# Kernel tuning notes

Measured on AMD Instinct MI355X. Metric: run time of the kernel, lower is better.

The kernel has to match this reference:

```python
import jax, jax.numpy as jnp
import numpy as np

PAD = 0  # vocab[PADDING]
T, B, S, E, H, V = 32, 32, 200, 512, 512, 50000


def setup_inputs() -> dict:
    key = jax.random.key(0)
    ks = jax.random.split(key, 16)
    u = lambda k, sh, s: jax.random.uniform(k, sh, jnp.float32, -s, s)
    lstm_s = 1.0 / np.sqrt(H)
    inp = {}
    inp["tgt_in"] = jax.random.randint(ks[0], (T, B), 0, V)
    inp["tgt_out"] = jax.random.randint(ks[1], (T, B), 0, V)
    inp["src_lens"] = jax.random.randint(ks[2], (B,), S // 2, S + 1)  # valid lengths >= 1
    inp["src_encodings"] = jax.random.normal(ks[3], (B, S, H), jnp.float32) * 0.1
    inp["last_state"] = jax.random.normal(ks[4], (1, B, H), jnp.float32) * 0.1
    inp["last_cell"] = jax.random.normal(ks[5], (1, B, H), jnp.float32) * 0.1
    inp["embed_table"] = jax.random.normal(ks[6], (V, E), jnp.float32) * 0.02
    in_sz = E + H  # input_feed=True
    inp["W_ih"] = u(ks[7], (4 * H, in_sz), lstm_s)
    inp["W_hh"] = u(ks[8], (4 * H, H), lstm_s)
    inp["b_ih"] = u(ks[9], (4 * H,), lstm_s)
    inp["b_hh"] = u(ks[10], (4 * H,), lstm_s)
    inp["W_attn"] = u(ks[11], (H, 2 * H), 1.0 / np.sqrt(2 * H))  # linear_out, no bias (dot attn)
    inp["W_gen"] = u(ks[12], (H, E + 2 * H), 1.0 / np.sqrt(E + 2 * H))
    inp["b_gen"] = u(ks[13], (H,), 1.0 / np.sqrt(E + 2 * H))
    inp["W_read"] = u(ks[14], (V, H), 1.0 / np.sqrt(H))  # readout, bias=False
    return inp


def reference(tgt_in, tgt_out, src_lens, src_encodings, last_state, last_cell,
              embed_table, W_ih, W_hh, b_ih, b_hh, W_attn, W_gen, b_gen, W_read):
    Bn = tgt_in.shape[1]
    Sn = src_encodings.shape[1]
    Hn = last_state.shape[-1]
    emb = embed_table[tgt_in]  # (T,B,E)
    len_mask = jnp.arange(Sn)[None, :] < src_lens[:, None]  # (B,S)
    h0 = last_state[0]
    c0 = last_cell[0]
    att0 = jnp.zeros((Bn, Hn), emb.dtype)  # att_tm1 init

    def step(carry, y_emb):
        h, c, att = carry
        x = jnp.concatenate([y_emb, att], axis=-1)  # input feed: (B,E+H)
        g = x @ W_ih.T + h @ W_hh.T + b_ih + b_hh  # (B,4H), torch gate order i,f,g,o
        i, f, gg, o = jnp.split(g, 4, axis=-1)
        c_new = jax.nn.sigmoid(f) * c + jax.nn.sigmoid(i) * jnp.tanh(gg)
        h_new = jax.nn.sigmoid(o) * jnp.tanh(c_new)
        # GlobalAttention (dot, softmax), query = last_state
        scores = jnp.einsum('bh,bsh->bs', h_new, src_encodings)  # (B,S)
        scores = jnp.where(len_mask, scores, -jnp.inf)
        alpha = jax.nn.softmax(scores, axis=-1)  # (B,S)
        ctx = jnp.einsum('bs,bsh->bh', alpha, src_encodings)  # (B,H)
        att_t = jnp.tanh(jnp.concatenate([ctx, h_new], axis=-1) @ W_attn.T)  # (B,H)
        cat_final = jnp.concatenate([y_emb, h_new, att_t], axis=-1)  # (B,E+2H)
        dec = jnp.tanh(cat_final @ W_gen.T + b_gen)  # (B,H)
        return (h_new, c_new, att_t), (dec, alpha)

    _, (decs, alphas) = jax.lax.scan(step, (h0, c0, att0), emb)  # decs: (T,B,H)
    logits = decs @ W_read.T  # (T,B,V)
    words_log_prob = jax.nn.log_softmax(logits, axis=-1)
    ys = jnp.argmax(words_log_prob, axis=-1)  # (T,B)
    words_mask = (tgt_out != PAD).astype(words_log_prob.dtype)
    word_losses = -jnp.take_along_axis(words_log_prob, tgt_out[..., None], axis=-1)[..., 0] * words_mask
    return word_losses, ys
```

## Files before the change

kernel.cpp:

```cpp
#include <hip/hip_runtime.h>
#include <math.h>

#define T_ 32
#define B_ 32
#define S_ 200
#define E_ 512
#define H_ 512
#define V_ 50000
#define VP_ 50176
#define G4_ 2048
#define NCH 196

using bf16x8 = __attribute__((ext_vector_type(8))) __bf16;
using f32x4  = __attribute__((ext_vector_type(4))) float;

__device__ __forceinline__ float sigf(float x) { return 1.f / (1.f + expf(-x)); }

__device__ __forceinline__ unsigned short f2bf(float v) {
    unsigned int x = __float_as_uint(v);
    return (unsigned short)((x + 0x7FFFu + ((x >> 16) & 1u)) >> 16);
}
__device__ __forceinline__ float bf2f(unsigned short b) {
    return __uint_as_float(((unsigned int)b) << 16);
}

__device__ __forceinline__ void async16(void* lds, const void* g) {
    __builtin_amdgcn_global_load_lds(
        (const __attribute__((address_space(1))) unsigned int*)g,
        (__attribute__((address_space(3))) unsigned int*)lds, 16, 0, 0);
}

__device__ __forceinline__ void g_store(float* p, float v) {
    __hip_atomic_store(p, v, __ATOMIC_RELAXED, __HIP_MEMORY_SCOPE_AGENT);
}
__device__ __forceinline__ float g_load(const float* p) {
    return __hip_atomic_load(p, __ATOMIC_RELAXED, __HIP_MEMORY_SCOPE_AGENT);
}

__device__ __forceinline__ void full_sync(int* bar, int ep) {
    __syncthreads();
    if (threadIdx.x == 0) {
        const int g = blockIdx.x & 7;
        int a = __hip_atomic_fetch_add(&bar[g * 32], 1, __ATOMIC_RELAXED, __HIP_MEMORY_SCOPE_AGENT);
        if (a == ep * 32 + 31) {
            int q = __hip_atomic_fetch_add(&bar[256], 1, __ATOMIC_RELAXED, __HIP_MEMORY_SCOPE_AGENT);
            if (q == ep * 8 + 7) {
                #pragma unroll
                for (int i = 0; i < 8; i++)
                    __hip_atomic_store(&bar[288 + i * 32], ep + 1, __ATOMIC_RELAXED, __HIP_MEMORY_SCOPE_AGENT);
            }
        }
        while (__hip_atomic_load(&bar[288 + g * 32], __ATOMIC_RELAXED, __HIP_MEMORY_SCOPE_AGENT) < ep + 1)
            __builtin_amdgcn_s_sleep(1);
    }
    __syncthreads();
}

__device__ __forceinline__ void sub_sync(int* bar, int bb, int t) {
    __syncthreads();
    if (threadIdx.x == 0) {
        __hip_atomic_fetch_add(&bar[544 + bb * 32], 1, __ATOMIC_RELAXED, __HIP_MEMORY_SCOPE_AGENT);
        while (__hip_atomic_load(&bar[544 + bb * 32], __ATOMIC_RELAXED, __HIP_MEMORY_SCOPE_AGENT) < (t + 1) * 8)
            __builtin_amdgcn_s_sleep(1);
    }
    __syncthreads();
}

__global__ __launch_bounds__(256) void k_init(const float* __restrict__ last_state,
                                              float* __restrict__ xT) {
    const int f = blockIdx.x * 256 + threadIdx.x;
    xT[f] = 0.f;
    const int k = f >> 5, b = f & 31;
    xT[32768 + f] = last_state[b * 512 + k];
}

#define CVT_R0 819200
#define CVT_R1 (CVT_R0 + 65536)
#define CVT_R2 (CVT_R1 + 262144)
#define CVT_R3 (CVT_R2 + 131072)
#define CVT_R4 (CVT_R3 + 196608)
__global__ __launch_bounds__(256) void k_cvt(const float* __restrict__ src,
                                             const float* __restrict__ Wattn,
                                             const float* __restrict__ Wih,
                                             const float* __restrict__ emb,
                                             const float* __restrict__ Wgen,
                                             const int* __restrict__ tgt_in,
                                             unsigned short* __restrict__ sh,
                                             unsigned short* __restrict__ sl,
                                             unsigned short* __restrict__ wah,
                                             unsigned short* __restrict__ wal,
                                             unsigned short* __restrict__ wih_h,
                                             unsigned short* __restrict__ wih_l,
                                             unsigned short* __restrict__ eh,
                                             unsigned short* __restrict__ el,
                                             unsigned short* __restrict__ wgh,
                                             unsigned short* __restrict__ wgl) {
    const int u = blockIdx.x * 256 + threadIdx.x;
    if (u >= CVT_R4) return;
    const float* sp;
    unsigned short *dh_, *dl_;
    size_t doff;
    if (u < CVT_R0) {
        sp = src + (size_t)u * 4;
        dh_ = sh; dl_ = sl; doff = (size_t)u * 4;
    } else if (u < CVT_R1) {
        const int idx = u - CVT_R0;
        const int k4 = idx & 127, n = idx >> 7;
        sp = Wattn + (size_t)n * 1024 + k4 * 4;
        dh_ = wah; dl_ = wal; doff = (size_t)n * 512 + k4 * 4;
    } else if (u < CVT_R2) {
        const int idx = u - CVT_R1;
        const int k4 = idx & 127, j = idx >> 7;
        sp = Wih + (size_t)j * 1024 + k4 * 4;
        dh_ = wih_h; dl_ = wih_l; doff = (size_t)j * 512 + k4 * 4;
    } else if (u < CVT_R3) {
        const int idx = u - CVT_R2;
        const int k4 = idx & 127, m = idx >> 7;
        sp = emb + (size_t)tgt_in[m] * 512 + k4 * 4;
        dh_ = eh; dl_ = el; doff = (size_t)m * 512 + k4 * 4;
    } else {
        const int idx = u - CVT_R3;
        const int n = idx / 384, k4 = idx - n * 384;
        sp = Wgen + (size_t)n * 1536 + k4 * 4;
        dh_ = wgh; dl_ = wgl; doff = (size_t)n * 1536 + k4 * 4;
    }
    const float4 v = *(const float4*)sp;
    const float vv[4] = {v.x, v.y, v.z, v.w};
    unsigned int hb[4], lb[4];
    #pragma unroll
    for (int e = 0; e < 4; e++) {
        hb[e] = f2bf(vv[e]);
        lb[e] = f2bf(vv[e] - bf2f((unsigned short)hb[e]));
    }
    *(uint2*)(dh_ + doff) = make_uint2(hb[0] | (hb[1] << 16), hb[2] | (hb[3] << 16));
    *(uint2*)(dl_ + doff) = make_uint2(lb[0] | (lb[1] << 16), lb[2] | (lb[3] << 16));
}

__global__ __launch_bounds__(256) void k_gbt(const unsigned short* __restrict__ Ah,
                                             const unsigned short* __restrict__ Al,
                                             const unsigned short* __restrict__ Bh,
                                             const unsigned short* __restrict__ Bl,
                                             const float* __restrict__ bih,
                                             const float* __restrict__ bhh,
                                             float* __restrict__ out,
                                             int nbn, int mode) {
    __shared__ __align__(16) unsigned short BhL[4][256][8];
    __shared__ __align__(16) unsigned short BlL[4][256][8];
    __shared__ __align__(16) unsigned short AhL[4][64][8];
    __shared__ __align__(16) unsigned short AlL[4][64][8];
    const int m0 = (blockIdx.x / nbn) * 64;
    const int n0 = (blockIdx.x % nbn) * 256;
    const int tid = threadIdx.x;
    const int lane = tid & 63, wid = tid >> 6;
    const int wr = wid >> 1, wc = wid & 1;
    const int l15 = lane & 15, lk = lane >> 4;

    f32x4 acc[2][8];
    #pragma unroll
    for (int mt = 0; mt < 2; mt++)
        #pragma unroll
        for (int nt = 0; nt < 8; nt++) acc[mt][nt] = {0.f, 0.f, 0.f, 0.f};

    for (int kc = 0; kc < 512; kc += 32) {
        {
            #pragma unroll
            for (int g = 0; g < 4; g++) {
                const size_t bo = (size_t)(n0 + tid) * 512 + kc + g * 8;
                *(uint4*)&BhL[g][tid][0] = *(const uint4*)(Bh + bo);
                *(uint4*)&BlL[g][tid][0] = *(const uint4*)(Bl + bo);
            }
        }
        {
            const int row = tid >> 2, g = tid & 3;
            const size_t ao = (size_t)(m0 + row) * 512 + kc + g * 8;
            *(uint4*)&AhL[g][row][0] = *(const uint4*)(Ah + ao);
            *(uint4*)&AlL[g][row][0] = *(const uint4*)(Al + ao);
        }
        __syncthreads();
        {
            bf16x8 afh[2], afl[2];
            #pragma unroll
            for (int mt = 0; mt < 2; mt++) {
                const int r = wr * 32 + mt * 16 + l15;
                afh[mt] = *(const bf16x8*)&AhL[lk][r][0];
                afl[mt] = *(const bf16x8*)&AlL[lk][r][0];
            }
            #pragma unroll
            for (int nt = 0; nt < 8; nt++) {
                const int nn = wc * 128 + nt * 16 + l15;
                bf16x8 bh = *(const bf16x8*)&BhL[lk][nn][0];
                bf16x8 bl = *(const bf16x8*)&BlL[lk][nn][0];
                #pragma unroll
                for (int mt = 0; mt < 2; mt++) {
                    acc[mt][nt] = __builtin_amdgcn_mfma_f32_16x16x32_bf16(afh[mt], bh, acc[mt][nt], 0, 0, 0);
                    acc[mt][nt] = __builtin_amdgcn_mfma_f32_16x16x32_bf16(afl[mt], bh, acc[mt][nt], 0, 0, 0);
                    acc[mt][nt] = __builtin_amdgcn_mfma_f32_16x16x32_bf16(afh[mt], bl, acc[mt][nt], 0, 0, 0);
                }
            }
        }
        __syncthreads();
    }
    #pragma unroll
    for (int mt = 0; mt < 2; mt++)
        #pragma unroll
        for (int reg = 0; reg < 4; reg++) {
            const int row = m0 + wr * 32 + mt * 16 + lk * 4 + reg;
            #pragma unroll
            for (int nt = 0; nt < 8; nt++) {
                const int col = n0 + wc * 128 + nt * 16 + l15;
                const float v = acc[mt][nt][reg];
                if (mode == 0) out[(size_t)row * 512 + col] = v;
                else           out[(size_t)col * 1024 + row] = v + bih[col] + bhh[col];
            }
        }
}

__global__ __launch_bounds__(256) void k_gbt_dec(const unsigned short* __restrict__ eh,
                                                 const unsigned short* __restrict__ el,
                                                 const unsigned short* __restrict__ hh,
                                                 const unsigned short* __restrict__ hl,
                                                 const unsigned short* __restrict__ ath,
                                                 const unsigned short* __restrict__ atl,
                                                 const unsigned short* __restrict__ wgh,
                                                 const unsigned short* __restrict__ wgl,
                                                 const float* __restrict__ bgen,
                                                 unsigned short* __restrict__ dhk,
                                                 unsigned short* __restrict__ dlk) {
    __shared__ __align__(16) unsigned short BhL[4][256][8];
    __shared__ __align__(16) unsigned short BlL[4][256][8];
    __shared__ __align__(16) unsigned short AhL[4][64][8];
    __shared__ __align__(16) unsigned short AlL[4][64][8];
    const int m0 = (blockIdx.x >> 1) * 64;
    const int n0 = (blockIdx.x & 1) * 256;
    const int tid = threadIdx.x;
    const int lane = tid & 63, wid = tid >> 6;
    const int wr = wid >> 1, wc = wid & 1;
    const int l15 = lane & 15, lk = lane >> 4;

    f32x4 acc[2][8];
    #pragma unroll
    for (int mt = 0; mt < 2; mt++)
        #pragma unroll
        for (int nt = 0; nt < 8; nt++) acc[mt][nt] = {0.f, 0.f, 0.f, 0.f};

    for (int kc = 0; kc < 1536; kc += 32) {
        const unsigned short *Ahp, *Alp;
        int ko;
        if (kc < 512)       { Ahp = eh;  Alp = el;  ko = kc; }
        else if (kc < 1024) { Ahp = hh;  Alp = hl;  ko = kc - 512; }
        else                { Ahp = ath; Alp = atl; ko = kc - 1024; }
        {
            #pragma unroll
            for (int g = 0; g < 4; g++) {
                const size_t bo = (size_t)(n0 + tid) * 1536 + kc + g * 8;
                *(uint4*)&BhL[g][tid][0] = *(const uint4*)(wgh + bo);
                *(uint4*)&BlL[g][tid][0] = *(const uint4*)(wgl + bo);
            }
        }
        {
            const int row = tid >> 2, g = tid & 3;
            const size_t ao = (size_t)(m0 + row) * 512 + ko + g * 8;
            *(uint4*)&AhL[g][row][0] = *(const uint4*)(Ahp + ao);
            *(uint4*)&AlL[g][row][0] = *(const uint4*)(Alp + ao);
        }
        __syncthreads();
        {
            bf16x8 afh[2], afl[2];
            #pragma unroll
            for (int mt = 0; mt < 2; mt++) {
                const int r = wr * 32 + mt * 16 + l15;
                afh[mt] = *(const bf16x8*)&AhL[lk][r][0];
                afl[mt] = *(const bf16x8*)&AlL[lk][r][0];
            }
            #pragma unroll
            for (int nt = 0; nt < 8; nt++) {
                const int nn = wc * 128 + nt * 16 + l15;
                bf16x8 bh = *(const bf16x8*)&BhL[lk][nn][0];
                bf16x8 bl = *(const bf16x8*)&BlL[lk][nn][0];
                #pragma unroll
                for (int mt = 0; mt < 2; mt++) {
                    acc[mt][nt] = __builtin_amdgcn_mfma_f32_16x16x32_bf16(afh[mt], bh, acc[mt][nt], 0, 0, 0);
                    acc[mt][nt] = __builtin_amdgcn_mfma_f32_16x16x32_bf16(afl[mt], bh, acc[mt][nt], 0, 0, 0);
                    acc[mt][nt] = __builtin_amdgcn_mfma_f32_16x16x32_bf16(afh[mt], bl, acc[mt][nt], 0, 0, 0);
                }
            }
        }
        __syncthreads();
    }
    #pragma unroll
    for (int mt = 0; mt < 2; mt++)
        #pragma unroll
        for (int reg = 0; reg < 4; reg++) {
            const int row = m0 + wr * 32 + mt * 16 + lk * 4 + reg;
            #pragma unroll
            for (int nt = 0; nt < 8; nt++) {
                const int col = n0 + wc * 128 + nt * 16 + l15;
                const float v = tanhf(acc[mt][nt][reg] + bgen[col]);
                const unsigned short hb = f2bf(v);
                const unsigned short lb = f2bf(v - bf2f(hb));
                const size_t ca = (size_t)(col >> 5) * 32768 + (size_t)(row >> 6) * 2048
                                + (size_t)(row & 63) * 32 + (col & 31);
                dhk[ca] = hb;
                dlk[ca] = lb;
            }
        }
}

__global__ __launch_bounds__(256) void k_g0(const int* __restrict__ tgt_in,
                                            const float* __restrict__ emb,
                                            const float* __restrict__ Wih,
                                            const float* __restrict__ bih,
                                            const float* __restrict__ bhh,
                                            float* __restrict__ G0T) {
    __shared__ float a_s[32][66];
    __shared__ float w_s[32][130];
    const int tid = threadIdx.x;
    const int m0 = blockIdx.x * 64, n0 = blockIdx.y * 128;
    const int mq = tid >> 5, nq = tid & 31;
    float acc[8][4] = {};
    for (int k0 = 0; k0 < 512; k0 += 32) {
        {
            const int mm = tid >> 2, kq = tid & 3, kk = kq * 8;
            const float* row = emb + (size_t)tgt_in[m0 + mm] * E_ + k0 + kk;
            float4 v0 = *(const float4*)(row);
            float4 v1 = *(const float4*)(row + 4);
            a_s[kk + 0][mm] = v0.x; a_s[kk + 1][mm] = v0.y;
            a_s[kk + 2][mm] = v0.z; a_s[kk + 3][mm] = v0.w;
            a_s[kk + 4][mm] = v1.x; a_s[kk + 5][mm] = v1.y;
            a_s[kk + 6][mm] = v1.z; a_s[kk + 7][mm] = v1.w;
        }
        {
            const int nn = tid >> 1, kq = tid & 1, kk = kq * 16;
            const float* row = Wih + (size_t)(n0 + nn) * 1024 + k0 + kk;
            #pragma unroll
            for (int u = 0; u < 4; u++) {
                float4 v = *(const float4*)(row + u * 4);
                w_s[kk + u * 4 + 0][nn] = v.x; w_s[kk + u * 4 + 1][nn] = v.y;
                w_s[kk + u * 4 + 2][nn] = v.z; w_s[kk + u * 4 + 3][nn] = v.w;
            }
        }
        __syncthreads();
        for (int k = 0; k < 32; k++) {
            float a[8], wv[4];
            #pragma unroll
            for (int i = 0; i < 8; i++) a[i] = a_s[k][mq + 8 * i];
            #pragma unroll
            for (int p = 0; p < 4; p++) wv[p] = w_s[k][nq + 32 * p];
            #pragma unroll
            for (int i = 0; i < 8; i++)
                #pragma unroll
                for (int p = 0; p < 4; p++) acc[i][p] += a[i] * wv[p];
        }
        __syncthreads();
    }
    #pragma unroll
    for (int i = 0; i < 8; i++) {
        const int m = m0 + mq + 8 * i;
        #pragma unroll
        for (int p = 0; p < 4; p++) {
            const int n = n0 + nq + 32 * p;
            G0T[(size_t)n * 1024 + m] = acc[i][p] + bih[n] + bhh[n];
        }
    }
}

__global__ __launch_bounds__(256) void k_u(const float* __restrict__ src,
                                           const float* __restrict__ Wattn,
                                           float* __restrict__ U) {
    __shared__ float a_s[32][66];
    __shared__ float w_s[32][130];
    const int tid = threadIdx.x;
    const int m0 = blockIdx.x * 64, n0 = blockIdx.y * 128;
    const int mq = tid >> 5, nq = tid & 31;
    float acc[8][4] = {};
    for (int k0 = 0; k0 < 512; k0 += 32) {
        {
            const int mm = tid >> 2, kq = tid & 3, kk = kq * 8;
            const float* row = src + (size_t)(m0 + mm) * 512 + k0 + kk;
            float4 v0 = *(const float4*)(row);
            float4 v1 = *(const float4*)(row + 4);
            a_s[kk + 0][mm] = v0.x; a_s[kk + 1][mm] = v0.y;
            a_s[kk + 2][mm] = v0.z; a_s[kk + 3][mm] = v0.w;
            a_s[kk + 4][mm] = v1.x; a_s[kk + 5][mm] = v1.y;
            a_s[kk + 6][mm] = v1.z; a_s[kk + 7][mm] = v1.w;
        }
        {
            const int nn = tid >> 1, kq = tid & 1, kk = kq * 16;
            const float* row = Wattn + (size_t)(n0 + nn) * 1024 + k0 + kk;
            #pragma unroll
            for (int u = 0; u < 4; u++) {
                float4 v = *(const float4*)(row + u * 4);
                w_s[kk + u * 4 + 0][nn] = v.x; w_s[kk + u * 4 + 1][nn] = v.y;
                w_s[kk + u * 4 + 2][nn] = v.z; w_s[kk + u * 4 + 3][nn] = v.w;
            }
        }
        __syncthreads();
        for (int k = 0; k < 32; k++) {
            float a[8], wv[4];
            #pragma unroll
            for (int i = 0; i < 8; i++) a[i] = a_s[k][mq + 8 * i];
            #pragma unroll
            for (int p = 0; p < 4; p++) wv[p] = w_s[k][nq + 32 * p];
            #pragma unroll
            for (int i = 0; i < 8; i++)
                #pragma unroll
                for (int p = 0; p < 4; p++) acc[i][p] += a[i] * wv[p];
        }
        __syncthreads();
    }
    #pragma unroll
    for (int i = 0; i < 8; i++) {
        const int m = m0 + mq + 8 * i;
        #pragma unroll
        for (int p = 0; p < 4; p++)
            U[(size_t)m * 512 + n0 + nq + 32 * p] = acc[i][p];
    }
}

__global__ __launch_bounds__(256) void k_tr(const float* __restrict__ Wattn,
                                            float* __restrict__ WaRT) {
    __shared__ float t_s[32][33];
    const int tid = threadIdx.x;
    const int bx = blockIdx.x, by = blockIdx.y;
    {
        const int jj = tid >> 3, kq = (tid & 7) * 4;
        float4 v = *(const float4*)(Wattn + (size_t)(by * 32 + jj) * 1024 + 512 + bx * 32 + kq);
        t_s[jj][kq + 0] = v.x; t_s[jj][kq + 1] = v.y;
        t_s[jj][kq + 2] = v.z; t_s[jj][kq + 3] = v.w;
    }
    __syncthreads();
    {
        const int kk = tid >> 3, jq = (tid & 7) * 4;
        float4 w;
        w.x = t_s[jq + 0][kk]; w.y = t_s[jq + 1][kk];
        w.z = t_s[jq + 2][kk]; w.w = t_s[jq + 3][kk];
        *(float4*)(WaRT + (size_t)(bx * 32 + kk) * 512 + by * 32 + jq) = w;
    }
}

__global__ __launch_bounds__(256) void k_wconv(const float* __restrict__ Wread,
                                               unsigned short* __restrict__ whk,
                                               unsigned short* __restrict__ wlk) {
    const size_t q = (size_t)blockIdx.x * 256 + threadIdx.x;
    const size_t k8 = q * 8;
    const int n = (int)(k8 >> 9);
    const int k = (int)(k8 & 511);
    if (n >= VP_) return;
    uint4 h4, l4;
    if (n < V_) {
        float4 p0 = *(const float4*)(Wread + (size_t)n * 512 + k);
        float4 p1 = *(const float4*)(Wread + (size_t)n * 512 + k + 4);
        float v[8] = {p0.x, p0.y, p0.z, p0.w, p1.x, p1.y, p1.z, p1.w};
        unsigned int hb[8], lb[8];
        #pragma unroll
        for (int e = 0; e < 8; e++) {
            hb[e] = f2bf(v[e]);
            lb[e] = f2bf(v[e] - bf2f((unsigned short)hb[e]));
        }
        h4 = make_uint4(hb[0] | (hb[1] << 16), hb[2] | (hb[3] << 16),
                        hb[4] | (hb[5] << 16), hb[6] | (hb[7] << 16));
        l4 = make_uint4(lb[0] | (lb[1] << 16), lb[2] | (lb[3] << 16),
                        lb[4] | (lb[5] << 16), lb[6] | (lb[7] << 16));
    } else {
        h4 = make_uint4(0, 0, 0, 0);
        l4 = make_uint4(0, 0, 0, 0);
    }
    const int lk = (k >> 3) & 3;
    const size_t dst = (size_t)(k >> 5) * ((size_t)VP_ * 32) + (size_t)n * 32
                     + (size_t)((lk ^ ((n >> 1) & 3)) * 8);
    *(uint4*)(whk + dst) = h4;
    *(uint4*)(wlk + dst) = l4;
}

__global__ __launch_bounds__(512) void k_scan(const float* __restrict__ G0T,
                                              const float* __restrict__ U,
                                              const float* __restrict__ WaRT,
                                              const float* __restrict__ Wih,
                                              const float* __restrict__ Whh,
                                              const float* __restrict__ src,
                                              const int* __restrict__ lens,
                                              const float* __restrict__ last_cell,
                                              float* __restrict__ xT,
                                              float* __restrict__ h_b,
                                              float* __restrict__ scb,
                                              float* __restrict__ h_hist,
                                              float* __restrict__ att_hist,
                                              unsigned short* __restrict__ hh,
                                              unsigned short* __restrict__ hl,
                                              unsigned short* __restrict__ ath,
                                              unsigned short* __restrict__ atl,
                                              int pre,
                                              int* __restrict__ bar) {
    __shared__ float Wl[8 * 1024];
    __shared__ float Ul[200 * 64];
    __shared__ float red_s[2048];
    __shared__ float gate_s[256];
    __shared__ float h_s[512];
    __shared__ float al[256];
    __shared__ float pr[512];

    const int blk = blockIdx.x, tid = threadIdx.x;
    const int u0 = blk * 2;
    const int bb = blk & 31, p = blk >> 5;

    for (int f = tid; f < 2048; f += 512) {
        const int r = f >> 8, k = (f & 255) * 4;
        const int j = (r >> 1) * 512 + u0 + (r & 1);
        float4 v;
        if (k < 512) v = *(const float4*)(Wih + (size_t)j * 1024 + 512 + k);
        else         v = *(const float4*)(Whh + (size_t)j * 512 + (k - 512));
        *(float4*)&Wl[r * 1024 + k] = v;
    }
    for (int f = tid; f < 3200; f += 512) {
        const int s = f >> 4, q = (f & 15) * 4;
        *(float4*)&Ul[s * 64 + q] = *(const float4*)(U + ((size_t)bb * S_ + s) * 512 + p * 64 + q);
    }
    float creg = (tid < 64) ? last_cell[(tid & 31) * 512 + u0 + (tid >> 5)] : 0.f;
    __syncthreads();

    const int w = tid >> 6, lane = tid & 63;
    const int hf = lane >> 5, b = lane & 31;
    const int len = lens[bb];

    for (int t = 0; t < T_; t++) {
        {
            const int hoff = ((t + 1) & 1) * 512;
            const int kbase = w * 128 + hf * 64;
            const float* xp = (kbase < 512)
                ? (xT + (size_t)kbase * 32 + b)
                : (xT + (size_t)(512 + hoff + (kbase - 512)) * 32 + b);
            float acc[8] = {};
            #pragma unroll
            for (int kk = 0; kk < 64; kk += 8) {
                float xv[8];
                #pragma unroll
                for (int i = 0; i < 8; i++)
                    xv[i] = g_load(xp + (size_t)(kk + i) * 32);
                #pragma unroll
                for (int r = 0; r < 8; r++) {
                    const float* wr = &Wl[r * 1024 + kbase + kk];
                    float s0 = xv[0] * wr[0] + xv[1] * wr[1] + xv[2] * wr[2] + xv[3] * wr[3];
                    float s1 = xv[4] * wr[4] + xv[5] * wr[5] + xv[6] * wr[6] + xv[7] * wr[7];
                    acc[r] += s0 + s1;
                }
            }
            #pragma unroll
            for (int r = 0; r < 8; r++) acc[r] += __shfl_xor(acc[r], 32);
            if (hf == 0) {
                #pragma unroll
                for (int r = 0; r < 8; r++) red_s[w * 256 + r * 32 + b] = acc[r];
            }
            __syncthreads();
            if (tid < 256) {
                const int r = tid >> 5, b2 = tid & 31;
                const int j = (r >> 1) * 512 + u0 + (r & 1);
                float g = G0T[(size_t)j * 1024 + t * 32 + b2];
                #pragma unroll
                for (int ww = 0; ww < 8; ww++) g += red_s[ww * 256 + r * 32 + b2];
                gate_s[r * 32 + b2] = g;
            }
            __syncthreads();
            if (tid < 64) {
                const int ui = tid >> 5, b2 = tid & 31, u = u0 + ui;
                const float gi = gate_s[(0 + ui) * 32 + b2];
                const float gf = gate_s[(2 + ui) * 32 + b2];
                const float gg = gate_s[(4 + ui) * 32 + b2];
                const float go = gate_s[(6 + ui) * 32 + b2];
                const float cn = sigf(gf) * creg + sigf(gi) * tanhf(gg);
                const float hn = sigf(go) * tanhf(cn);
                creg = cn;
                g_store(&xT[(size_t)(512 + (t & 1) * 512 + u) * 32 + b2], hn);
                g_store(&h_b[b2 * 512 + u], hn);
                h_hist[((size_t)t * B_ + b2) * 512 + u] = hn;
                if (pre) {
                    const unsigned short hb2 = f2bf(hn);
                    const size_t ho = ((size_t)t * B_ + b2) * 512 + u;
                    hh[ho] = hb2;
                    hl[ho] = f2bf(hn - bf2f(hb2));
                }
            }
        }
        full_sync(bar, 2 * t);

        {
            h_s[tid] = g_load(&h_b[bb * 512 + tid]);
            __syncthreads();
            for (int i = w; i < 25; i += 8) {
                const int s = p * 25 + i;
                const float* sr = src + ((size_t)bb * S_ + s) * 512;
                const float4 x0 = *(const float4*)(sr + lane * 4);
                const float4 x1 = *(const float4*)(sr + 256 + lane * 4);
                const float4 h0 = *(const float4*)(&h_s[lane * 4]);
                const float4 h1 = *(const float4*)(&h_s[256 + lane * 4]);
                float a = x0.x * h0.x + x0.y * h0.y + x0.z * h0.z + x0.w * h0.w
                        + x1.x * h1.x + x1.y * h1.y + x1.z * h1.z + x1.w * h1.w;
                #pragma unroll
                for (int mk = 1; mk < 64; mk <<= 1) a += __shfl_xor(a, mk);
                if (lane == 0) g_store(&scb[bb * 256 + s], (s < len) ? a : -INFINITY);
            }
        }
        sub_sync(bar, bb, t);

        {
            if (tid < 64) {
                const float v0 = g_load(&scb[bb * 256 + tid]);
                const float v1 = g_load(&scb[bb * 256 + 64 + tid]);
                const float v2 = g_load(&scb[bb * 256 + 128 + tid]);
                const float v3 = (tid < 8) ? g_load(&scb[bb * 256 + 192 + tid]) : -INFINITY;
                float m = fmaxf(fmaxf(v0, v1), fmaxf(v2, v3));
                #pragma unroll
                for (int mk = 1; mk < 64; mk <<= 1) m = fmaxf(m, __shfl_xor(m, mk));
                const float e0 = expf(v0 - m), e1 = expf(v1 - m), e2 = expf(v2 - m);
                const float e3 = (tid < 8) ? expf(v3 - m) : 0.f;
                float sum = (e0 + e1) + (e2 + e3);
                #pragma unroll
                for (int mk = 1; mk < 64; mk <<= 1) sum += __shfl_xor(sum, mk);
                const float inv = 1.f / sum;
                al[tid] = e0 * inv; al[64 + tid] = e1 * inv; al[128 + tid] = e2 * inv;
                if (tid < 8) al[192 + tid] = e3 * inv;
            }
            __syncthreads();
            const int jl = tid & 63, sg = tid >> 6;
            float uacc = 0.f;
            #pragma unroll 5
            for (int s = sg * 25; s < sg * 25 + 25; s++)
                uacc += al[s] * Ul[s * 64 + jl];
            const float* wc0 = WaRT + (size_t)(sg * 64) * 512 + p * 64 + jl;
            const float* hp = &h_s[sg * 64];
            float c0 = 0.f, c1 = 0.f;
            #pragma unroll 8
            for (int kk = 0; kk < 64; kk += 2) {
                c0 += hp[kk] * wc0[(size_t)kk * 512];
                c1 += hp[kk + 1] * wc0[(size_t)(kk + 1) * 512];
            }
            pr[tid] = uacc + c0 + c1;
            __syncthreads();
            if (tid < 64) {
                float tot = 0.f;
                #pragma unroll
                for (int sgg = 0; sgg < 8; sgg++) tot += pr[sgg * 64 + tid];
                const float a = tanhf(tot);
                g_store(&xT[(size_t)(p * 64 + tid) * 32 + bb], a);
                att_hist[((size_t)t * B_ + bb) * 512 + p * 64 + tid] = a;
                if (pre) {
                    const unsigned short ab = f2bf(a);
                    const size_t ao = ((size_t)t * B_ + bb) * 512 + p * 64 + tid;
                    ath[ao] = ab;
                    atl[ao] = f2bf(a - bf2f(ab));
                }
            }
        }
        full_sync(bar, 2 * t + 1);
    }
}

__global__ __launch_bounds__(256) void k_dec(const int* __restrict__ tgt_in,
                                             const float* __restrict__ emb,
                                             const float* __restrict__ h_hist,
                                             const float* __restrict__ att_hist,
                                             const float* __restrict__ Wgen,
                                             const float* __restrict__ bgen,
                                             unsigned short* __restrict__ dh,
                                             unsigned short* __restrict__ dl) {
    __shared__ float a_s[32][66];
    __shared__ float w_s[32][130];
    const int tid = threadIdx.x;
    const int m0 = blockIdx.x * 64, n0 = blockIdx.y * 128;
    const int mq = tid >> 5, nq = tid & 31;
    float acc[8][4] = {};
    for (int k0 = 0; k0 < 1536; k0 += 32) {
        {
            const int mm = tid >> 2, kq = tid & 3, kk = kq * 8;
            const int m = m0 + mm;
            const float* row;
            if (k0 < 512)       row = emb + (size_t)tgt_in[m] * E_ + k0;
            else if (k0 < 1024) row = h_hist + (size_t)m * 512 + (k0 - 512);
            else                row = att_hist + (size_t)m * 512 + (k0 - 1024);
            row += kk;
            float4 v0 = *(const float4*)(row);
            float4 v1 = *(const float4*)(row + 4);
            a_s[kk + 0][mm] = v0.x; a_s[kk + 1][mm] = v0.y;
            a_s[kk + 2][mm] = v0.z; a_s[kk + 3][mm] = v0.w;
            a_s[kk + 4][mm] = v1.x; a_s[kk + 5][mm] = v1.y;
            a_s[kk + 6][mm] = v1.z; a_s[kk + 7][mm] = v1.w;
        }
        {
            const int nn = tid >> 1, kq = tid & 1, kk = kq * 16;
            const float* row = Wgen + (size_t)(n0 + nn) * 1536 + k0 + kk;
            #pragma unroll
            for (int u = 0; u < 4; u++) {
                float4 v = *(const float4*)(row + u * 4);
                w_s[kk + u * 4 + 0][nn] = v.x; w_s[kk + u * 4 + 1][nn] = v.y;
                w_s[kk + u * 4 + 2][nn] = v.z; w_s[kk + u * 4 + 3][nn] = v.w;
            }
        }
        __syncthreads();
        for (int k = 0; k < 32; k++) {
            float a[8], wv[4];
            #pragma unroll
            for (int i = 0; i < 8; i++) a[i] = a_s[k][mq + 8 * i];
            #pragma unroll
            for (int pq = 0; pq < 4; pq++) wv[pq] = w_s[k][nq + 32 * pq];
            #pragma unroll
            for (int i = 0; i < 8; i++)
                #pragma unroll
                for (int pq = 0; pq < 4; pq++) acc[i][pq] += a[i] * wv[pq];
        }
        __syncthreads();
    }
    #pragma unroll
    for (int i = 0; i < 8; i++) {
        const int m = m0 + mq + 8 * i;
        #pragma unroll
        for (int pq = 0; pq < 4; pq++) {
            const int n = n0 + nq + 32 * pq;
            const float v = tanhf(acc[i][pq] + bgen[n]);
            const unsigned short hb = f2bf(v);
            dh[(size_t)m * 512 + n] = hb;
            dl[(size_t)m * 512 + n] = f2bf(v - bf2f(hb));
        }
    }
}

__global__ __launch_bounds__(256) void k_read_pre(const unsigned short* __restrict__ dhk,
                                                  const unsigned short* __restrict__ dlk,
                                                  const unsigned short* __restrict__ whk,
                                                  const unsigned short* __restrict__ wlk,
                                                  const int* __restrict__ tgt_out,
                                                  float4* __restrict__ part,
                                                  float* __restrict__ tgt_logit) {
    __shared__ __align__(16) unsigned short BhL[8192];
    __shared__ __align__(16) unsigned short BlL[8192];
    __shared__ float ep_max[64][2];
    __shared__ int   ep_idx[64][2];
    __shared__ float ep_fin[64];
    __shared__ int   ep_fidx[64];
    __shared__ float ep_sum[64][2];

    const int xcd = blockIdx.x & 7;
    const int idx = blockIdx.x >> 3;
    const int mi  = idx & 15;
    const int group = idx >> 4;
    const int ch = group * 8 + xcd;
    if (ch >= NCH) return;
    const int m0 = mi * 64, n0 = ch * 256;

    const int tid = threadIdx.x;
    const int lane = tid & 63, wid = tid >> 6;
    const int wr = wid >> 1, wc = wid & 1;
    const int l15 = lane & 15, lk = lane >> 4;

    f32x4 acc[2][8];
    #pragma unroll
    for (int mt = 0; mt < 2; mt++)
        #pragma unroll
        for (int nt = 0; nt < 8; nt++) acc[mt][nt] = {0.f, 0.f, 0.f, 0.f};

    const unsigned short* bh_src = whk + (size_t)n0 * 32;
    const unsigned short* bl_src = wlk + (size_t)n0 * 32;
    const unsigned short* ah_base = dhk + (size_t)(m0 >> 6) * 2048 + lk * 8;
    const unsigned short* al_base = dlk + (size_t)(m0 >> 6) * 2048 + lk * 8;

    for (int kc = 0; kc < 16; kc++) {
        {
            const size_t cb = (size_t)kc * ((size_t)VP_ * 32);
            const char* gh = (const char*)(bh_src + cb);
            const char* gl = (const char*)(bl_src + cb);
            #pragma unroll
            for (int c = 0; c < 4; c++) {
                const int ob = wid * 4096 + c * 1024;
                async16((char*)BhL + ob, gh + ob + lane * 16);
                async16((char*)BlL + ob, gl + ob + lane * 16);
            }
        }
        bf16x8 afh[2], afl[2];
        {
            const unsigned short* ah = ah_base + (size_t)kc * 32768;
            const unsigned short* al = al_base + (size_t)kc * 32768;
            #pragma unroll
            for (int mt = 0; mt < 2; mt++) {
                const int r = wr * 32 + mt * 16 + l15;
                afh[mt] = *(const bf16x8*)(ah + r * 32);
                afl[mt] = *(const bf16x8*)(al + r * 32);
            }
        }
        __syncthreads();
        #pragma unroll
        for (int nt = 0; nt < 8; nt++) {
            const int nn = wc * 128 + nt * 16 + l15;
            const int bo = nn * 32 + ((lk ^ ((nn >> 1) & 3)) * 8);
            bf16x8 bh = *(const bf16x8*)&BhL[bo];
            bf16x8 bl = *(const bf16x8*)&BlL[bo];
            #pragma unroll
            for (int mt = 0; mt < 2; mt++) {
                acc[mt][nt] = __builtin_amdgcn_mfma_f32_16x16x32_bf16(afh[mt], bh, acc[mt][nt], 0, 0, 0);
                acc[mt][nt] = __builtin_amdgcn_mfma_f32_16x16x32_bf16(afl[mt], bh, acc[mt][nt], 0, 0, 0);
                acc[mt][nt] = __builtin_amdgcn_mfma_f32_16x16x32_bf16(afh[mt], bl, acc[mt][nt], 0, 0, 0);
            }
        }
        __syncthreads();
    }

    #pragma unroll
    for (int mt = 0; mt < 2; mt++)
        #pragma unroll
        for (int reg = 0; reg < 4; reg++) {
            float bv = -INFINITY; int bi = 0x7fffffff;
            #pragma unroll
            for (int nt = 0; nt < 8; nt++) {
                const int n = n0 + wc * 128 + nt * 16 + l15;
                const float v = (n < V_) ? acc[mt][nt][reg] : -INFINITY;
                if (v > bv || (v == bv && n < bi)) { bv = v; bi = n; }
            }
            #pragma unroll
            for (int mk = 1; mk < 16; mk <<= 1) {
                const float ov = __shfl_xor(bv, mk);
                const int oi = __shfl_xor(bi, mk);
                if (ov > bv || (ov == bv && oi < bi)) { bv = ov; bi = oi; }
            }
            if (l15 == 0) {
                const int rl = wr * 32 + mt * 16 + lk * 4 + reg;
                ep_max[rl][wc] = bv; ep_idx[rl][wc] = bi;
            }
        }
    __syncthreads();
    if (tid < 64) {
        const float a = ep_max[tid][0], b = ep_max[tid][1];
        const int ia = ep_idx[tid][0], ib = ep_idx[tid][1];
        const bool tb = (b > a) || (b == a && ib < ia);
        ep_fin[tid] = tb ? b : a; ep_fidx[tid] = tb ? ib : ia;
    }
    __syncthreads();
    #pragma unroll
    for (int mt = 0; mt < 2; mt++)
        #pragma unroll
        for (int reg = 0; reg < 4; reg++) {
            const int rl = wr * 32 + mt * 16 + lk * 4 + reg;
            const float M = ep_fin[rl];
            const int rel = tgt_out[m0 + rl] - n0;
            float se = 0.f;
            #pragma unroll
            for (int nt = 0; nt < 8; nt++) {
                const int nl = wc * 128 + nt * 16 + l15;
                if (n0 + nl < V_) {
                    const float v = acc[mt][nt][reg];
                    se += expf(v - M);
                    if (nl == rel) tgt_logit[m0 + rl] = v;
                }
            }
            #pragma unroll
            for (int mk = 1; mk < 16; mk <<= 1) se += __shfl_xor(se, mk);
            if (l15 == 0) ep_sum[rl][wc] = se;
        }
    __syncthreads();
    if (tid < 64) {
        part[(size_t)(m0 + tid) * NCH + ch] =
            make_float4(ep_fin[tid], ep_sum[tid][0] + ep_sum[tid][1],
                        __int_as_float(ep_fidx[tid]), 0.f);
    }
}

__global__ __launch_bounds__(256) void k_read(const unsigned short* __restrict__ dh,
                                              const unsigned short* __restrict__ dl,
                                              const float* __restrict__ Wread,
                                              const int* __restrict__ tgt_out,
                                              float4* __restrict__ part,
                                              float* __restrict__ tgt_logit) {
    __shared__ __align__(16) unsigned short Bh[4][256][8];
    __shared__ __align__(16) unsigned short Bl[4][256][8];
    __shared__ __align__(16) unsigned short Ah[4][64][8];
    __shared__ __align__(16) unsigned short Alo[4][64][8];
    __shared__ float ep_max[64][2];
    __shared__ int   ep_idx[64][2];
    __shared__ float ep_fin[64];
    __shared__ int   ep_fidx[64];
    __shared__ float ep_sum[64][2];

    const int xcd = blockIdx.x & 7;
    const int idx = blockIdx.x >> 3;
    const int mi  = idx & 15;
    const int group = idx >> 4;
    const int ch = group * 8 + xcd;
    if (ch >= NCH) return;
    const int m0 = mi * 64, n0 = ch * 256;

    const int tid = threadIdx.x;
    const int lane = tid & 63, wid = tid >> 6;
    const int wr = wid >> 1, wc = wid & 1;
    const int l15 = lane & 15, lk = lane >> 4;

    f32x4 acc[2][8];
    #pragma unroll
    for (int mt = 0; mt < 2; mt++)
        #pragma unroll
        for (int nt = 0; nt < 8; nt++) acc[mt][nt] = {0.f, 0.f, 0.f, 0.f};

    for (int kc = 0; kc < 512; kc += 32) {
        {
            const int n = n0 + tid;
            const float* row = Wread + (size_t)n * 512 + kc;
            #pragma unroll
            for (int g = 0; g < 4; g++) {
                uint4 h4, l4;
                if (n < V_) {
                    float4 p0 = *(const float4*)(row + g * 8);
                    float4 p1 = *(const float4*)(row + g * 8 + 4);
                    float v[8] = {p0.x, p0.y, p0.z, p0.w, p1.x, p1.y, p1.z, p1.w};
                    unsigned int hb[8], lb[8];
                    #pragma unroll
                    for (int e = 0; e < 8; e++) {
                        hb[e] = f2bf(v[e]);
                        lb[e] = f2bf(v[e] - bf2f((unsigned short)hb[e]));
                    }
                    h4 = make_uint4(hb[0] | (hb[1] << 16), hb[2] | (hb[3] << 16),
                                    hb[4] | (hb[5] << 16), hb[6] | (hb[7] << 16));
                    l4 = make_uint4(lb[0] | (lb[1] << 16), lb[2] | (lb[3] << 16),
                                    lb[4] | (lb[5] << 16), lb[6] | (lb[7] << 16));
                } else {
                    h4 = make_uint4(0, 0, 0, 0);
                    l4 = make_uint4(0, 0, 0, 0);
                }
                *(uint4*)&Bh[g][tid][0] = h4;
                *(uint4*)&Bl[g][tid][0] = l4;
            }
        }
        {
            const int row = tid >> 2, g = tid & 3;
            *(uint4*)&Ah[g][row][0]  = *(const uint4*)(dh + (size_t)(m0 + row) * 512 + kc + g * 8);
            *(uint4*)&Alo[g][row][0] = *(const uint4*)(dl + (size_t)(m0 + row) * 512 + kc + g * 8);
        }
        __syncthreads();
        {
            bf16x8 afh[2], afl[2];
            #pragma unroll
            for (int mt = 0; mt < 2; mt++) {
                const int r = wr * 32 + mt * 16 + l15;
                afh[mt] = *(const bf16x8*)&Ah[lk][r][0];
                afl[mt] = *(const bf16x8*)&Alo[lk][r][0];
            }
            #pragma unroll
            for (int nt = 0; nt < 8; nt++) {
                const int nn = wc * 128 + nt * 16 + l15;
                bf16x8 bh = *(const bf16x8*)&Bh[lk][nn][0];
                bf16x8 bl = *(const bf16x8*)&Bl[lk][nn][0];
                #pragma unroll
                for (int mt = 0; mt < 2; mt++) {
                    acc[mt][nt] = __builtin_amdgcn_mfma_f32_16x16x32_bf16(afh[mt], bh, acc[mt][nt], 0, 0, 0);
                    acc[mt][nt] = __builtin_amdgcn_mfma_f32_16x16x32_bf16(afl[mt], bh, acc[mt][nt], 0, 0, 0);
                    acc[mt][nt] = __builtin_amdgcn_mfma_f32_16x16x32_bf16(afh[mt], bl, acc[mt][nt], 0, 0, 0);
                }
            }
        }
        __syncthreads();
    }

    #pragma unroll
    for (int mt = 0; mt < 2; mt++)
        #pragma unroll
        for (int reg = 0; reg < 4; reg++) {
            float bv = -INFINITY; int bi = 0x7fffffff;
            #pragma unroll
            for (int nt = 0; nt < 8; nt++) {
                const int n = n0 + wc * 128 + nt * 16 + l15;
                const float v = (n < V_) ? acc[mt][nt][reg] : -INFINITY;
                if (v > bv || (v == bv && n < bi)) { bv = v; bi = n; }
            }
            #pragma unroll
            for (int mk = 1; mk < 16; mk <<= 1) {
                const float ov = __shfl_xor(bv, mk);
                const int oi = __shfl_xor(bi, mk);
                if (ov > bv || (ov == bv && oi < bi)) { bv = ov; bi = oi; }
            }
            if (l15 == 0) {
                const int rl = wr * 32 + mt * 16 + lk * 4 + reg;
                ep_max[rl][wc] = bv; ep_idx[rl][wc] = bi;
            }
        }
    __syncthreads();
    if (tid < 64) {
        const float a = ep_max[tid][0], b = ep_max[tid][1];
        const int ia = ep_idx[tid][0], ib = ep_idx[tid][1];
        const bool tb = (b > a) || (b == a && ib < ia);
        ep_fin[tid] = tb ? b : a; ep_fidx[tid] = tb ? ib : ia;
    }
    __syncthreads();
    #pragma unroll
    for (int mt = 0; mt < 2; mt++)
        #pragma unroll
        for (int reg = 0; reg < 4; reg++) {
            const int rl = wr * 32 + mt * 16 + lk * 4 + reg;
            const float M = ep_fin[rl];
            const int rel = tgt_out[m0 + rl] - n0;
            float se = 0.f;
            #pragma unroll
            for (int nt = 0; nt < 8; nt++) {
                const int nl = wc * 128 + nt * 16 + l15;
                if (n0 + nl < V_) {
                    const float v = acc[mt][nt][reg];
                    se += expf(v - M);
                    if (nl == rel) tgt_logit[m0 + rl] = v;
                }
            }
            #pragma unroll
            for (int mk = 1; mk < 16; mk <<= 1) se += __shfl_xor(se, mk);
            if (l15 == 0) ep_sum[rl][wc] = se;
        }
    __syncthreads();
    if (tid < 64) {
        part[(size_t)(m0 + tid) * NCH + ch] =
            make_float4(ep_fin[tid], ep_sum[tid][0] + ep_sum[tid][1],
                        __int_as_float(ep_fidx[tid]), 0.f);
    }
}

__global__ __launch_bounds__(256) void k_merge(const float4* __restrict__ part,
                                               const float* __restrict__ tgt_logit,
                                               const int* __restrict__ tgt_out,
                                               float* __restrict__ out) {
    const int tid = threadIdx.x;
    const int w = tid >> 6, lane = tid & 63;
    const int row = blockIdx.x * 4 + w;
    float bm = -INFINITY; int bi = 0x7fffffff;
    for (int ch = lane; ch < NCH; ch += 64) {
        const float4 p = part[(size_t)row * NCH + ch];
        const int pi = __float_as_int(p.z);
        if (p.x > bm || (p.x == bm && pi < bi)) { bm = p.x; bi = pi; }
    }
    #pragma unroll
    for (int mk = 1; mk < 64; mk <<= 1) {
        const float ov = __shfl_xor(bm, mk);
        const int oi = __shfl_xor(bi, mk);
        if (ov > bm || (ov == bm && oi < bi)) { bm = ov; bi = oi; }
    }
    float sum = 0.f;
    for (int ch = lane; ch < NCH; ch += 64) {
        const float4 p = part[(size_t)row * NCH + ch];
        sum += p.y * expf(p.x - bm);
    }
    #pragma unroll
    for (int mk = 1; mk < 64; mk <<= 1) sum += __shfl_xor(sum, mk);
    if (lane == 0) {
        const float lse = bm + logf(sum);
        const int tg = tgt_out[row];
        const float loss = (tg != 0) ? (lse - tgt_logit[row]) : 0.f;
        out[row] = loss;
        out[1024 + row] = (float)bi;
    }
}

extern "C" void kernel_launch(void* const* d_in, const int* in_sizes, int n_in,
                              void* d_out, int out_size, void* d_ws, size_t ws_size,
                              hipStream_t stream) {
    const int* tgt_in = (const int*)d_in[0];
    const int* tgt_out = (const int*)d_in[1];
    const int* src_lens = (const int*)d_in[2];
    const float* src = (const float*)d_in[3];
    const float* last_state = (const float*)d_in[4];
    const float* last_cell = (const float*)d_in[5];
    const float* emb = (const float*)d_in[6];
    const float* Wih = (const float*)d_in[7];
    const float* Whh = (const float*)d_in[8];
    const float* bih = (const float*)d_in[9];
    const float* bhh = (const float*)d_in[10];
    const float* Wattn = (const float*)d_in[11];
    const float* Wgen = (const float*)d_in[12];
    const float* bgen = (const float*)d_in[13];
    const float* Wread = (const float*)d_in[14];
    float* out = (float*)d_out;

    float* ws = (float*)d_ws;
    float* G0T      = ws;
    float* U        = G0T + 2097152;
    float* WaRT     = U + 3276800;
    unsigned short* dh  = (unsigned short*)(WaRT + 262144);
    unsigned short* dl  = dh + 524288;
    unsigned short* dhk = dl + 524288;
    unsigned short* dlk = dhk + 524288;
    float* h_hist   = (float*)(dlk + 524288);
    float* att_hist = h_hist + 524288;
    float* xT       = att_hist + 524288;
    float* h_b      = xT + 49152;
    float* scb      = h_b + 16384;
    float4* part    = (float4*)(scb + 8192);
    float* tgtl     = ((float*)part) + 802816;
    int* bar        = (int*)(tgtl + 1024);
    unsigned short* whk = (unsigned short*)(bar + 2048);
    unsigned short* wlk = whk + (size_t)VP_ * 512;
    unsigned short* sh    = wlk + (size_t)VP_ * 512;
    unsigned short* sl    = sh + 3276800;
    unsigned short* wah   = sl + 3276800;
    unsigned short* wal   = wah + 262144;
    unsigned short* wih_h = wal + 262144;
    unsigned short* wih_l = wih_h + 1048576;
    unsigned short* eh    = wih_l + 1048576;
    unsigned short* el    = eh + 524288;
    unsigned short* wgh   = el + 524288;
    unsigned short* wgl   = wgh + 786432;
    unsigned short* hh    = wgl + 786432;
    unsigned short* hl    = hh + 524288;
    unsigned short* ath   = hl + 524288;
    unsigned short* atl   = ath + 524288;

    const size_t need = (size_t)((char*)(atl + 524288) - (char*)ws);
    const int pre = (ws_size >= need) ? 1 : 0;

    hipMemsetAsync(bar, 0, 8192, stream);

    k_init<<<64, 256, 0, stream>>>(last_state, xT);
    if (pre) {
        k_cvt<<<(CVT_R4 + 255) / 256, 256, 0, stream>>>(src, Wattn, Wih, emb, Wgen, tgt_in,
                                                        sh, sl, wah, wal, wih_h, wih_l,
                                                        eh, el, wgh, wgl);
        k_gbt<<<200, 256, 0, stream>>>(sh, sl, wah, wal, nullptr, nullptr, U, 2, 0);
        k_gbt<<<128, 256, 0, stream>>>(eh, el, wih_h, wih_l, bih, bhh, G0T, 8, 1);
    } else {
        k_g0<<<dim3(16, 16), 256, 0, stream>>>(tgt_in, emb, Wih, bih, bhh, G0T);
        k_u<<<dim3(100, 4), 256, 0, stream>>>(src, Wattn, U);
    }
    k_tr<<<dim3(16, 16), 256, 0, stream>>>(Wattn, WaRT);
    if (pre)
        k_wconv<<<12544, 256, 0, stream>>>(Wread, whk, wlk);

    k_scan<<<256, 512, 0, stream>>>(G0T, U, WaRT, Wih, Whh, src, src_lens, last_cell,
                                    xT, h_b, scb, h_hist, att_hist,
                                    hh, hl, ath, atl, pre, bar);

    if (pre) {
        k_gbt_dec<<<32, 256, 0, stream>>>(eh, el, hh, hl, ath, atl, wgh, wgl, bgen, dhk, dlk);
        k_read_pre<<<3200, 256, 0, stream>>>(dhk, dlk, whk, wlk, tgt_out, part, tgtl);
    } else {
        k_dec<<<dim3(16, 4), 256, 0, stream>>>(tgt_in, emb, h_hist, att_hist, Wgen, bgen, dh, dl);
        k_read<<<3200, 256, 0, stream>>>(dh, dl, Wread, tgt_out, part, tgtl);
    }
    k_merge<<<256, 256, 0, stream>>>(part, tgtl, tgt_out, out);
}
```

Measured before the change: 900.9 us.

## Double-buffer readout weight tiles and split rows across eight waves

The readout GEMM kernel now uses 512 threads (8 waves), each wave owning 16 rows instead of 32, which halves per-thread accumulators. The weight tile loads are double-buffered in shared memory, so the next k-chunk is fetched asynchronously while the current one feeds the MFMAs, and one barrier per iteration is removed. The aim is to hide global-load latency and raise occupancy, at the cost of twice the LDS footprint and more waves re-reading the same B fragments.

```diff
diff --git a/kernel.cpp b/kernel.cpp
--- a/kernel.cpp
+++ b/kernel.cpp
@@ -722,15 +722,15 @@
     }
 }
 
-__global__ __launch_bounds__(256) void k_read_pre(const unsigned short* __restrict__ dhk,
+__global__ __launch_bounds__(512) void k_read_pre(const unsigned short* __restrict__ dhk,
                                                   const unsigned short* __restrict__ dlk,
                                                   const unsigned short* __restrict__ whk,
                                                   const unsigned short* __restrict__ wlk,
                                                   const int* __restrict__ tgt_out,
                                                   float4* __restrict__ part,
                                                   float* __restrict__ tgt_logit) {
-    __shared__ __align__(16) unsigned short BhL[8192];
-    __shared__ __align__(16) unsigned short BlL[8192];
+    __shared__ __align__(16) unsigned short BhL[2][8192];
+    __shared__ __align__(16) unsigned short BlL[2][8192];
     __shared__ float ep_max[64][2];
     __shared__ int   ep_idx[64][2];
     __shared__ float ep_fin[64];
@@ -750,79 +750,81 @@
     const int wr = wid >> 1, wc = wid & 1;
     const int l15 = lane & 15, lk = lane >> 4;
 
-    f32x4 acc[2][8];
-    #pragma unroll
-    for (int mt = 0; mt < 2; mt++)
-        #pragma unroll
-        for (int nt = 0; nt < 8; nt++) acc[mt][nt] = {0.f, 0.f, 0.f, 0.f};
+    f32x4 acc[8];
+    #pragma unroll
+    for (int nt = 0; nt < 8; nt++) acc[nt] = {0.f, 0.f, 0.f, 0.f};
 
     const unsigned short* bh_src = whk + (size_t)n0 * 32;
     const unsigned short* bl_src = wlk + (size_t)n0 * 32;
     const unsigned short* ah_base = dhk + (size_t)(m0 >> 6) * 2048 + lk * 8;
     const unsigned short* al_base = dlk + (size_t)(m0 >> 6) * 2048 + lk * 8;
 
+    {
+        const char* gh = (const char*)bh_src;
+        const char* gl = (const char*)bl_src;
+        #pragma unroll
+        for (int c = 0; c < 2; c++) {
+            const int ob = wid * 2048 + c * 1024;
+            async16((char*)&BhL[0][0] + ob, gh + ob + lane * 16);
+            async16((char*)&BlL[0][0] + ob, gl + ob + lane * 16);
+        }
+    }
+    __syncthreads();
+
     for (int kc = 0; kc < 16; kc++) {
-        {
-            const size_t cb = (size_t)kc * ((size_t)VP_ * 32);
+        const int cur = kc & 1;
+        bf16x8 afh, afl;
+        {
+            const unsigned short* ah = ah_base + (size_t)kc * 32768;
+            const unsigned short* al = al_base + (size_t)kc * 32768;
+            const int r = wr * 16 + l15;
+            afh = *(const bf16x8*)(ah + r * 32);
+            afl = *(const bf16x8*)(al + r * 32);
+        }
+        if (kc < 15) {
+            const size_t cb = (size_t)(kc + 1) * ((size_t)VP_ * 32);
             const char* gh = (const char*)(bh_src + cb);
             const char* gl = (const char*)(bl_src + cb);
             #pragma unroll
-            for (int c = 0; c < 4; c++) {
-                const int ob = wid * 4096 + c * 1024;
-                async16((char*)BhL + ob, gh + ob + lane * 16);
-                async16((char*)BlL + ob, gl + ob + lane * 16);
-            }
-        }
-        bf16x8 afh[2], afl[2];
-        {
-            const unsigned short* ah = ah_base + (size_t)kc * 32768;
-            const unsigned short* al = al_base + (size_t)kc * 32768;
-            #pragma unroll
-            for (int mt = 0; mt < 2; mt++) {
-                const int r = wr * 32 + mt * 16 + l15;
-                afh[mt] = *(const bf16x8*)(ah + r * 32);
-                afl[mt] = *(const bf16x8*)(al + r * 32);
-            }
-        }
-        __syncthreads();
+            for (int c = 0; c < 2; c++) {
+                const int ob = wid * 2048 + c * 1024;
+                async16((char*)&BhL[cur ^ 1][0] + ob, gh + ob + lane * 16);
+                async16((char*)&BlL[cur ^ 1][0] + ob, gl + ob + lane * 16);
+            }
+        }
         #pragma unroll
         for (int nt = 0; nt < 8; nt++) {
             const int nn = wc * 128 + nt * 16 + l15;
             const int bo = nn * 32 + ((lk ^ ((nn >> 1) & 3)) * 8);
-            bf16x8 bh = *(const bf16x8*)&BhL[bo];
-            bf16x8 bl = *(const bf16x8*)&BlL[bo];
-            #pragma unroll
-            for (int mt = 0; mt < 2; mt++) {
-                acc[mt][nt] = __builtin_amdgcn_mfma_f32_16x16x32_bf16(afh[mt], bh, acc[mt][nt], 0, 0, 0);
-                acc[mt][nt] = __builtin_amdgcn_mfma_f32_16x16x32_bf16(afl[mt], bh, acc[mt][nt], 0, 0, 0);
-                acc[mt][nt] = __builtin_amdgcn_mfma_f32_16x16x32_bf16(afh[mt], bl, acc[mt][nt], 0, 0, 0);
-            }
-        }
-        __syncthreads();
-    }
-
-    #pragma unroll
-    for (int mt = 0; mt < 2; mt++)
-        #pragma unroll
-        for (int reg = 0; reg < 4; reg++) {
-            float bv = -INFINITY; int bi = 0x7fffffff;
-            #pragma unroll
-            for (int nt = 0; nt < 8; nt++) {
-                const int n = n0 + wc * 128 + nt * 16 + l15;
-                const float v = (n < V_) ? acc[mt][nt][reg] : -INFINITY;
-                if (v > bv || (v == bv && n < bi)) { bv = v; bi = n; }
-            }
-            #pragma unroll
-            for (int mk = 1; mk < 16; mk <<= 1) {
-                const float ov = __shfl_xor(bv, mk);
-                const int oi = __shfl_xor(bi, mk);
-                if (ov > bv || (ov == bv && oi < bi)) { bv = ov; bi = oi; }
-            }
-            if (l15 == 0) {
-                const int rl = wr * 32 + mt * 16 + lk * 4 + reg;
-                ep_max[rl][wc] = bv; ep_idx[rl][wc] = bi;
-            }
-        }
+            bf16x8 bh = *(const bf16x8*)&BhL[cur][bo];
+            bf16x8 bl = *(const bf16x8*)&BlL[cur][bo];
+            acc[nt] = __builtin_amdgcn_mfma_f32_16x16x32_bf16(afh, bh, acc[nt], 0, 0, 0);
+            acc[nt] = __builtin_amdgcn_mfma_f32_16x16x32_bf16(afl, bh, acc[nt], 0, 0, 0);
+            acc[nt] = __builtin_amdgcn_mfma_f32_16x16x32_bf16(afh, bl, acc[nt], 0, 0, 0);
+        }
+        __syncthreads();
+    }
+
+    #pragma unroll
+    for (int reg = 0; reg < 4; reg++) {
+        float bv = -INFINITY; int bi = 0x7fffffff;
+        #pragma unroll
+        for (int nt = 0; nt < 8; nt++) {
+            const int n = n0 + wc * 128 + nt * 16 + l15;
+            const float v = (n < V_) ? acc[nt][reg] : -INFINITY;
+            if (v > bv || (v == bv && n < bi)) { bv = v; bi = n; }
+        }
+        #pragma unroll
+        for (int mk = 1; mk < 16; mk <<= 1) {
+            const float ov = __shfl_xor(bv, mk);
+            const int oi = __shfl_xor(bi, mk);
+            if (ov > bv || (ov == bv && oi < bi)) { bv = ov; bi = oi; }
+        }
+        if (l15 == 0) {
+            const int rl = wr * 16 + lk * 4 + reg;
+            ep_max[rl][wc] = bv; ep_idx[rl][wc] = bi;
+        }
+    }
     __syncthreads();
     if (tid < 64) {
         const float a = ep_max[tid][0], b = ep_max[tid][1];
@@ -832,26 +834,24 @@
     }
     __syncthreads();
     #pragma unroll
-    for (int mt = 0; mt < 2; mt++)
-        #pragma unroll
-        for (int reg = 0; reg < 4; reg++) {
-            const int rl = wr * 32 + mt * 16 + lk * 4 + reg;
-            const float M = ep_fin[rl];
-            const int rel = tgt_out[m0 + rl] - n0;
-            float se = 0.f;
-            #pragma unroll
-            for (int nt = 0; nt < 8; nt++) {
-                const int nl = wc * 128 + nt * 16 + l15;
-                if (n0 + nl < V_) {
-                    const float v = acc[mt][nt][reg];
-                    se += expf(v - M);
-                    if (nl == rel) tgt_logit[m0 + rl] = v;
-                }
-            }
-            #pragma unroll
-            for (int mk = 1; mk < 16; mk <<= 1) se += __shfl_xor(se, mk);
-            if (l15 == 0) ep_sum[rl][wc] = se;
-        }
+    for (int reg = 0; reg < 4; reg++) {
+        const int rl = wr * 16 + lk * 4 + reg;
+        const float M = ep_fin[rl];
+        const int rel = tgt_out[m0 + rl] - n0;
+        float se = 0.f;
+        #pragma unroll
+        for (int nt = 0; nt < 8; nt++) {
+            const int nl = wc * 128 + nt * 16 + l15;
+            if (n0 + nl < V_) {
+                const float v = acc[nt][reg];
+                se += expf(v - M);
+                if (nl == rel) tgt_logit[m0 + rl] = v;
+            }
+        }
+        #pragma unroll
+        for (int mk = 1; mk < 16; mk <<= 1) se += __shfl_xor(se, mk);
+        if (l15 == 0) ep_sum[rl][wc] = se;
+    }
     __syncthreads();
     if (tid < 64) {
         part[(size_t)(m0 + tid) * NCH + ch] =
@@ -1127,7 +1127,7 @@
 
     if (pre) {
         k_gbt_dec<<<32, 256, 0, stream>>>(eh, el, hh, hl, ath, atl, wgh, wgl, bgen, dhk, dlk);
-        k_read_pre<<<3200, 256, 0, stream>>>(dhk, dlk, whk, wlk, tgt_out, part, tgtl);
+        k_read_pre<<<3200, 512, 0, stream>>>(dhk, dlk, whk, wlk, tgt_out, part, tgtl);
     } else {
         k_dec<<<dim3(16, 4), 256, 0, stream>>>(tgt_in, emb, h_hist, att_hist, Wgen, bgen, dh, dl);
         k_read<<<3200, 256, 0, stream>>>(dh, dl, Wread, tgt_out, part, tgtl);
```

After: 875.1 us. 1.03x faster.
